# Kernel optimization log

Hardware: AMD Instinct MI355X
Metric: run time of the kernel (lower is better)

The kernel has to match this reference:

```python
import jax, jax.numpy as jnp
import numpy as np

GROUPS = 8
EPS = 1e-5


def setup_inputs() -> dict:
    key = jax.random.key(0)
    ks = jax.random.split(key, 7)
    b, c, h, w = 32, 256, 32, 32
    x = jax.random.normal(ks[0], (b, c, h, w), dtype=jnp.float32)
    gn_weight = jax.random.normal(ks[1], (c,), dtype=jnp.float32) * 0.02 + 1.0
    gn_bias = jax.random.normal(ks[2], (c,), dtype=jnp.float32) * 0.02
    w_qkv = jax.random.normal(ks[3], (3 * c, c), dtype=jnp.float32) / np.sqrt(c)
    b_qkv = jax.random.normal(ks[4], (3 * c,), dtype=jnp.float32) * 0.01
    w_out = jax.random.normal(ks[5], (c, c), dtype=jnp.float32) / np.sqrt(c)
    b_out = jax.random.normal(ks[6], (c,), dtype=jnp.float32) * 0.01
    return {"x": x, "gn_weight": gn_weight, "gn_bias": gn_bias,
            "w_qkv": w_qkv, "b_qkv": b_qkv, "w_out": w_out, "b_out": b_out}


def group_norm(x, weight, bias):
    b, c, h, w = x.shape
    xg = x.reshape(b, GROUPS, c // GROUPS, h, w)
    mean = jnp.mean(xg, axis=(2, 3, 4), keepdims=True)
    var = jnp.var(xg, axis=(2, 3, 4), keepdims=True)
    xg = (xg - mean) * jax.lax.rsqrt(var + EPS)
    x = xg.reshape(b, c, h, w)
    return x * weight[None, :, None, None] + bias[None, :, None, None]


def reference(x, gn_weight, gn_bias, w_qkv, b_qkv, w_out, b_out):
    b, c, h, w = x.shape
    x_norm = group_norm(x, gn_weight, gn_bias)
    # 1x1 conv == channel matmul: (b, 3c, h, w)
    qkv = jnp.einsum('oc,bchw->bohw', w_qkv, x_norm) + b_qkv[None, :, None, None]
    q, k, v = jnp.split(qkv, 3, axis=1)
    hw = h * w
    q = q.reshape(b, c, hw)  # used transposed: (b, hw, c)
    k = k.reshape(b, c, hw)
    v = v.reshape(b, c, hw)
    scale = 1.0 / jnp.sqrt(jnp.float32(c))
    attn = jax.nn.softmax(jnp.einsum('bcs,bct->bst', q, k) * scale, axis=-1)  # (b, hw, hw)
    out = jnp.einsum('bst,bct->bcs', attn, v).reshape(b, c, h, w)
    out = jnp.einsum('oc,bchw->bohw', w_out, out) + b_out[None, :, None, None]
    return out + x
```

## Files before the change

kernel.cpp:

```cpp
#include <hip/hip_runtime.h>
#include <hip/hip_bf16.h>


typedef __bf16 bf16x8 __attribute__((ext_vector_type(8)));
typedef __bf16 bf16x4 __attribute__((ext_vector_type(4)));
typedef float f32x4 __attribute__((ext_vector_type(4)));
typedef float f32x16 __attribute__((ext_vector_type(16)));

#define MFMA16(a, b, c) __builtin_amdgcn_mfma_f32_16x16x32_bf16(a, b, c, 0, 0, 0)
#define MFMA32(a, b, c) __builtin_amdgcn_mfma_f32_32x32x16_bf16(a, b, c, 0, 0, 0)

__global__ __launch_bounds__(256) void wconv_kernel(const float* __restrict__ wqkv,
                                                    const float* __restrict__ wout,
                                                    __bf16* __restrict__ wbf) {
    int idx = (blockIdx.x * 256 + threadIdx.x) * 8;
    const float* src = (idx < 196608) ? (wqkv + idx) : (wout + (idx - 196608));
    float4 v0 = *(const float4*)src;
    float4 v1 = *(const float4*)(src + 4);
    bf16x8 o;
    o[0] = (__bf16)v0.x; o[1] = (__bf16)v0.y; o[2] = (__bf16)v0.z; o[3] = (__bf16)v0.w;
    o[4] = (__bf16)v1.x; o[5] = (__bf16)v1.y; o[6] = (__bf16)v1.z; o[7] = (__bf16)v1.w;
    *(bf16x8*)&wbf[idx] = o;
}

__global__ __launch_bounds__(512) void gn_kernel(const float* __restrict__ x,
                                                 const float* __restrict__ gw,
                                                 const float* __restrict__ gb,
                                                 __bf16* __restrict__ xnT) {
    __shared__ float red[16];
    __shared__ float stats[2];
    __shared__ __bf16 Lds[512][40];
    const int b = blockIdx.x >> 3, g = blockIdx.x & 7;
    const size_t base = ((size_t)b * 256 + g * 32) * 1024;
    const float* xp = x + base;
    const int t = threadIdx.x;

    float s = 0.f, s2 = 0.f;
    #pragma unroll
    for (int i = 0; i < 8; i++) {
        int j = i * 512 + t;
        float4 v0 = *(const float4*)(xp + (size_t)j * 8);
        float4 v1 = *(const float4*)(xp + (size_t)j * 8 + 4);
        s  += v0.x + v0.y + v0.z + v0.w + v1.x + v1.y + v1.z + v1.w;
        s2 += v0.x*v0.x + v0.y*v0.y + v0.z*v0.z + v0.w*v0.w
            + v1.x*v1.x + v1.y*v1.y + v1.z*v1.z + v1.w*v1.w;
    }
    #pragma unroll
    for (int o = 32; o > 0; o >>= 1) { s += __shfl_down(s, o, 64); s2 += __shfl_down(s2, o, 64); }
    const int wv = t >> 6;
    if ((t & 63) == 0) { red[wv * 2] = s; red[wv * 2 + 1] = s2; }
    __syncthreads();
    if (t == 0) {
        float ts = 0.f, ts2 = 0.f;
        for (int w = 0; w < 8; w++) { ts += red[w * 2]; ts2 += red[w * 2 + 1]; }
        float mean = ts / 32768.f;
        float var = ts2 / 32768.f - mean * mean;
        stats[0] = mean; stats[1] = rsqrtf(var + 1e-5f);
    }
    __syncthreads();
    const float mean = stats[0], inv = stats[1];

    const int c = t >> 4;
    const int so = (t & 15) * 2;
    const float ga = gw[g * 32 + c], be = gb[g * 32 + c];

    for (int chunk = 0; chunk < 1024; chunk += 512) {
        #pragma unroll
        for (int i = 0; i < 16; i++) {
            int sl = so + i * 32;
            float2 v = *(const float2*)(xp + (size_t)c * 1024 + chunk + sl);
            Lds[sl][c]     = (__bf16)((v.x - mean) * inv * ga + be);
            Lds[sl + 1][c] = (__bf16)((v.y - mean) * inv * ga + be);
        }
        __syncthreads();
        {
            int sl = t;
            #pragma unroll
            for (int u = 0; u < 4; u++) {
                bf16x8 vv = *(const bf16x8*)&Lds[sl][u * 8];
                *(bf16x8*)&xnT[((size_t)b * 1024 + chunk + sl) * 256 + g * 32 + u * 8] = vv;
            }
        }
        __syncthreads();
    }
}

#define GEMM64_BODY(ArowBase_, BrowBase_)                                               \
    f32x4 acc[4][4] = {};                                                               \
    const int r_ = t >> 1, kc_ = (t & 1) * 32;                                          \
    bf16x8 pa[4], pb[4];                                                                \
    _Pragma("unroll")                                                                   \
    for (int u = 0; u < 4; u++) {                                                       \
        pa[u] = *(const bf16x8*)&(ArowBase_)[(size_t)r_ * 256 + kc_ + u * 8];           \
        pb[u] = *(const bf16x8*)&(BrowBase_)[(size_t)r_ * 256 + kc_ + u * 8];           \
    }                                                                                   \
    for (int kk = 0; kk < 256; kk += 64) {                                              \
        _Pragma("unroll")                                                               \
        for (int u = 0; u < 4; u++) {                                                   \
            *(bf16x8*)&As[r_][kc_ + u * 8] = pa[u];                                     \
            *(bf16x8*)&Bs[r_][kc_ + u * 8] = pb[u];                                     \
        }                                                                               \
        __syncthreads();                                                                \
        if (kk < 192) {                                                                 \
            _Pragma("unroll")                                                           \
            for (int u = 0; u < 4; u++) {                                               \
                pa[u] = *(const bf16x8*)&(ArowBase_)[(size_t)r_ * 256 + kk + 64 + kc_ + u * 8]; \
                pb[u] = *(const bf16x8*)&(BrowBase_)[(size_t)r_ * 256 + kk + 64 + kc_ + u * 8]; \
            }                                                                           \
        }                                                                               \
        _Pragma("unroll")                                                               \
        for (int kh = 0; kh < 2; kh++) {                                                \
            bf16x8 af[4], bfv[4];                                                       \
            _Pragma("unroll")                                                           \
            for (int im = 0; im < 4; im++)                                              \
                af[im] = *(const bf16x8*)&As[wm + im * 16 + l16][kh * 32 + quad * 8];   \
            _Pragma("unroll")                                                           \
            for (int in = 0; in < 4; in++)                                              \
                bfv[in] = *(const bf16x8*)&Bs[wn + in * 16 + l16][kh * 32 + quad * 8];  \
            _Pragma("unroll")                                                           \
            for (int im = 0; im < 4; im++)                                              \
                _Pragma("unroll")                                                       \
                for (int in = 0; in < 4; in++)                                          \
                    acc[im][in] = MFMA16(af[im], bfv[in], acc[im][in]);                 \
        }                                                                               \
        __syncthreads();                                                                \
    }

__global__ __launch_bounds__(256) void qkv_gemm(const __bf16* __restrict__ wbf,
                                                const float* __restrict__ bias,
                                                const __bf16* __restrict__ xnT,
                                                __bf16* __restrict__ qtr,
                                                __bf16* __restrict__ ktr,
                                                __bf16* __restrict__ vbuf) {
    __shared__ __bf16 As[128][72];
    __shared__ __bf16 Bs[128][72];
    const int b = blockIdx.z;
    const int n0 = blockIdx.x * 128, m0 = blockIdx.y * 128;
    const int t = threadIdx.x;
    const int wave = t >> 6, lane = t & 63, quad = lane >> 4, l16 = lane & 15;
    const int wm = (wave & 1) * 64, wn = (wave >> 1) * 64;
    const __bf16* arow = wbf + (size_t)m0 * 256;
    const __bf16* brow = xnT + ((size_t)b * 1024 + n0) * 256;

    GEMM64_BODY(arow, brow)

    #pragma unroll
    for (int im = 0; im < 4; im++) {
        #pragma unroll
        for (int in = 0; in < 4; in++) {
            int sg = n0 + wn + in * 16 + l16;
            int ob = m0 + wm + im * 16 + quad * 4;
            if (m0 < 512) {
                bf16x4 ov;
                #pragma unroll
                for (int r = 0; r < 4; r++) ov[r] = (__bf16)(acc[im][in][r] + bias[ob + r]);
                __bf16* dst = (m0 < 256) ? &qtr[((size_t)b * 1024 + sg) * 256 + ob]
                                         : &ktr[((size_t)b * 1024 + sg) * 256 + (ob - 256)];
                *(bf16x4*)dst = ov;
            } else {
                #pragma unroll
                for (int r = 0; r < 4; r++) {
                    float val = acc[im][in][r] + bias[ob + r];
                    vbuf[((size_t)b * 256 + (ob - 512 + r)) * 1024 + sg] = (__bf16)val;
                }
            }
        }
    }
}

__global__ __launch_bounds__(512, 2) void attn_kernel(const __bf16* __restrict__ qtr,
                                                      const __bf16* __restrict__ ktr,
                                                      const __bf16* __restrict__ vbuf,
                                                      __bf16* __restrict__ aoT) {
    __shared__ __bf16 Kt[2][32][260];
    __shared__ __bf16 Vs[2][256][36];
    __shared__ __bf16 Pl[4][32][72];
    __shared__ float Lred[4][2][32];
    const int b = blockIdx.x;
    const int tid = threadIdx.x;
    const int wave = tid >> 6, lane = tid & 63, half = lane >> 5, l31 = lane & 31;
    const int pair = wave & 3, th = wave >> 2;
    const int s0 = blockIdx.y * 128 + pair * 32;
    const float kscale = 0.09016844f;

    bf16x8 aq[16];
    #pragma unroll
    for (int ks = 0; ks < 16; ks++)
        aq[ks] = *(const bf16x8*)&qtr[((size_t)b * 1024 + s0 + l31) * 256 + ks * 16 + half * 8];

    const int k_row = tid >> 3;
    const int k_cb  = (tid & 7) * 8;
    const int v_c   = tid >> 1;
    const int v_th  = tid & 1;
    const size_t kbase = (size_t)b * 1024 * 256;
    const size_t vbase = (size_t)b * 256 * 1024;

    float l_part[16] = {};
    f32x16 o_acc[4] = {};

    for (int it = 0; it < 16; it++) {
        const int t0 = it * 64;
        #pragma unroll
        for (int u = 0; u < 4; u++) {
            bf16x8 kv = *(const bf16x8*)&ktr[kbase + (size_t)(t0 + k_row) * 256 + k_cb + u * 64];
            *(bf16x8*)&Kt[k_row >> 5][k_row & 31][k_cb + u * 64] = kv;
        }
        #pragma unroll
        for (int u = 0; u < 4; u++) {
            bf16x8 vv = *(const bf16x8*)&vbuf[vbase + (size_t)v_c * 1024 + t0 + v_th * 32 + u * 8];
            *(bf16x8*)&Vs[v_th][v_c][u * 8] = vv;
        }
        __syncthreads();

        f32x16 sc_a = {}, sc_b = {};
        #pragma unroll
        for (int ks = 0; ks < 8; ks++) {
            bf16x8 bk0 = *(const bf16x8*)&Kt[th][l31][ks * 16 + half * 8];
            bf16x8 bk1 = *(const bf16x8*)&Kt[th][l31][(ks + 8) * 16 + half * 8];
            sc_a = MFMA32(aq[ks], bk0, sc_a);
            sc_b = MFMA32(aq[ks + 8], bk1, sc_b);
        }
        #pragma unroll
        for (int r = 0; r < 16; r++) {
            float p = exp2f((sc_a[r] + sc_b[r]) * kscale);
            l_part[r] += p;
            int row = (r & 3) + 8 * (r >> 2) + 4 * half;
            Pl[pair][row][th * 32 + l31] = (__bf16)p;
        }
        __syncthreads();

        bf16x8 ap[4];
        #pragma unroll
        for (int kc = 0; kc < 4; kc++)
            ap[kc] = *(const bf16x8*)&Pl[pair][l31][kc * 16 + half * 8];
        #pragma unroll
        for (int n = 0; n < 4; n++) {
            int c = th * 128 + n * 32 + l31;
            #pragma unroll
            for (int kc = 0; kc < 4; kc++) {
                bf16x8 bv = *(const bf16x8*)&Vs[kc >> 1][c][(kc & 1) * 16 + half * 8];
                o_acc[n] = MFMA32(ap[kc], bv, o_acc[n]);
            }
        }
        __syncthreads();
    }

    float lsum[16];
    #pragma unroll
    for (int r = 0; r < 16; r++) {
        float l = l_part[r];
        #pragma unroll
        for (int m = 16; m > 0; m >>= 1) l += __shfl_xor(l, m, 32);
        lsum[r] = l;
        if (l31 == 0) {
            int row = (r & 3) + 8 * (r >> 2) + 4 * half;
            Lred[pair][th][row] = l;
        }
    }
    __syncthreads();
    #pragma unroll
    for (int r = 0; r < 16; r++) {
        int row = (r & 3) + 8 * (r >> 2) + 4 * half;
        float rinv = 1.0f / (lsum[r] + Lred[pair][1 - th][row]);
        #pragma unroll
        for (int n = 0; n < 4; n++) {
            int c = th * 128 + n * 32 + l31;
            aoT[((size_t)b * 1024 + s0 + row) * 256 + c] = (__bf16)(o_acc[n][r] * rinv);
        }
    }
}

__global__ __launch_bounds__(256) void proj_gemm(const __bf16* __restrict__ wbf_out,
                                                 const float* __restrict__ bias,
                                                 const __bf16* __restrict__ aoT,
                                                 const float* __restrict__ resid,
                                                 float* __restrict__ Out) {
    __shared__ __bf16 As[128][72];
    __shared__ __bf16 Bs[128][72];
    const int b = blockIdx.z;
    const int n0 = blockIdx.x * 128, m0 = blockIdx.y * 128;
    const int t = threadIdx.x;
    const int wave = t >> 6, lane = t & 63, quad = lane >> 4, l16 = lane & 15;
    const int wm = (wave & 1) * 64, wn = (wave >> 1) * 64;
    const __bf16* arow = wbf_out + (size_t)m0 * 256;
    const __bf16* brow = aoT + ((size_t)b * 1024 + n0) * 256;

    GEMM64_BODY(arow, brow)

    #pragma unroll
    for (int im = 0; im < 4; im++) {
        #pragma unroll
        for (int in = 0; in < 4; in++) {
            int sg = n0 + wn + in * 16 + l16;
            int ob = m0 + wm + im * 16 + quad * 4;
            #pragma unroll
            for (int r = 0; r < 4; r++) {
                int o = ob + r;
                size_t idx = ((size_t)b * 256 + o) * 1024 + sg;
                Out[idx] = acc[im][in][r] + bias[o] + resid[idx];
            }
        }
    }
}

extern "C" void kernel_launch(void* const* d_in, const int* in_sizes, int n_in,
                              void* d_out, int out_size, void* d_ws, size_t ws_size,
                              hipStream_t stream) {
    const float* x    = (const float*)d_in[0];
    const float* gw   = (const float*)d_in[1];
    const float* gb   = (const float*)d_in[2];
    const float* wqkv = (const float*)d_in[3];
    const float* bqkv = (const float*)d_in[4];
    const float* wout = (const float*)d_in[5];
    const float* bout = (const float*)d_in[6];
    float* out = (float*)d_out;

    const size_t T16 = (size_t)32 * 1024 * 256;
    __bf16* xnT  = (__bf16*)d_ws;
    __bf16* qtr  = xnT + T16;
    __bf16* ktr  = qtr + T16;
    __bf16* vbuf = ktr + T16;
    __bf16* aoT  = vbuf + T16;
    __bf16* wbf  = aoT + T16;

    wconv_kernel<<<dim3(128), 256, 0, stream>>>(wqkv, wout, wbf);
    gn_kernel<<<dim3(256), 512, 0, stream>>>(x, gw, gb, xnT);
    qkv_gemm<<<dim3(8, 6, 32), 256, 0, stream>>>(wbf, bqkv, xnT, qtr, ktr, vbuf);
    attn_kernel<<<dim3(32, 8), 512, 0, stream>>>(qtr, ktr, vbuf, aoT);
    proj_gemm<<<dim3(8, 2, 32), 256, 0, stream>>>(wbf + 196608, bout, aoT, x, out);
}
```

Before: 210.8 us.

## Fuse weight cast into groupnorm, stage GEMM epilogues through LDS, prefetch K/V

Folds the weight fp32-to-bf16 conversion into the groupnorm kernel, which removes one launch. The Q/K epilogue of the QKV GEMM and the projection epilogue are staged through shared memory so global stores (and residual loads) become coalesced 16-byte vectors. The attention loop prefetches the next K/V tile into registers while computing the current one, and raises wave priority around the MFMA sections. The added LDS round-trips and barriers in the epilogues, plus higher register pressure from the prefetch in attention, are the costs.

Measured after the change: 194.2 us. 7.9% less time.

```diff
diff --git a/kernel.cpp b/kernel.cpp
--- a/kernel.cpp
+++ b/kernel.cpp
@@ -4,29 +4,20 @@
 
 typedef __bf16 bf16x8 __attribute__((ext_vector_type(8)));
 typedef __bf16 bf16x4 __attribute__((ext_vector_type(4)));
+typedef __bf16 bf16x2 __attribute__((ext_vector_type(2)));
 typedef float f32x4 __attribute__((ext_vector_type(4)));
 typedef float f32x16 __attribute__((ext_vector_type(16)));
 
 #define MFMA16(a, b, c) __builtin_amdgcn_mfma_f32_16x16x32_bf16(a, b, c, 0, 0, 0)
 #define MFMA32(a, b, c) __builtin_amdgcn_mfma_f32_32x32x16_bf16(a, b, c, 0, 0, 0)
-
-__global__ __launch_bounds__(256) void wconv_kernel(const float* __restrict__ wqkv,
-                                                    const float* __restrict__ wout,
-                                                    __bf16* __restrict__ wbf) {
-    int idx = (blockIdx.x * 256 + threadIdx.x) * 8;
-    const float* src = (idx < 196608) ? (wqkv + idx) : (wout + (idx - 196608));
-    float4 v0 = *(const float4*)src;
-    float4 v1 = *(const float4*)(src + 4);
-    bf16x8 o;
-    o[0] = (__bf16)v0.x; o[1] = (__bf16)v0.y; o[2] = (__bf16)v0.z; o[3] = (__bf16)v0.w;
-    o[4] = (__bf16)v1.x; o[5] = (__bf16)v1.y; o[6] = (__bf16)v1.z; o[7] = (__bf16)v1.w;
-    *(bf16x8*)&wbf[idx] = o;
-}
 
 __global__ __launch_bounds__(512) void gn_kernel(const float* __restrict__ x,
                                                  const float* __restrict__ gw,
                                                  const float* __restrict__ gb,
-                                                 __bf16* __restrict__ xnT) {
+                                                 __bf16* __restrict__ xnT,
+                                                 const float* __restrict__ wqkv,
+                                                 const float* __restrict__ wout,
+                                                 __bf16* __restrict__ wbf) {
     __shared__ float red[16];
     __shared__ float stats[2];
     __shared__ __bf16 Lds[512][40];
@@ -34,6 +25,15 @@
     const size_t base = ((size_t)b * 256 + g * 32) * 1024;
     const float* xp = x + base;
     const int t = threadIdx.x;
+
+    {
+        int widx = (blockIdx.x * 512 + t) * 2;
+        const float* wsrc = (widx < 196608) ? (wqkv + widx) : (wout + (widx - 196608));
+        float2 wv = *(const float2*)wsrc;
+        bf16x2 wo;
+        wo[0] = (__bf16)wv.x; wo[1] = (__bf16)wv.y;
+        *(bf16x2*)&wbf[widx] = wo;
+    }
 
     float s = 0.f, s2 = 0.f;
     #pragma unroll
@@ -132,8 +132,10 @@
                                                 __bf16* __restrict__ qtr,
                                                 __bf16* __restrict__ ktr,
                                                 __bf16* __restrict__ vbuf) {
-    __shared__ __bf16 As[128][72];
-    __shared__ __bf16 Bs[128][72];
+    __shared__ union {
+        struct { __bf16 A[128][72]; __bf16 B[128][72]; } g;
+        __bf16 ct[128][136];
+    } sm;
     const int b = blockIdx.z;
     const int n0 = blockIdx.x * 128, m0 = blockIdx.y * 128;
     const int t = threadIdx.x;
@@ -141,23 +143,46 @@
     const int wm = (wave & 1) * 64, wn = (wave >> 1) * 64;
     const __bf16* arow = wbf + (size_t)m0 * 256;
     const __bf16* brow = xnT + ((size_t)b * 1024 + n0) * 256;
+    auto As = sm.g.A;
+    auto Bs = sm.g.B;
 
     GEMM64_BODY(arow, brow)
 
-    #pragma unroll
-    for (int im = 0; im < 4; im++) {
-        #pragma unroll
-        for (int in = 0; in < 4; in++) {
-            int sg = n0 + wn + in * 16 + l16;
-            int ob = m0 + wm + im * 16 + quad * 4;
-            if (m0 < 512) {
+    if (m0 < 512) {
+        #pragma unroll
+        for (int im = 0; im < 4; im++) {
+            #pragma unroll
+            for (int in = 0; in < 4; in++) {
+                int ob = m0 + wm + im * 16 + quad * 4;
                 bf16x4 ov;
                 #pragma unroll
                 for (int r = 0; r < 4; r++) ov[r] = (__bf16)(acc[im][in][r] + bias[ob + r]);
-                __bf16* dst = (m0 < 256) ? &qtr[((size_t)b * 1024 + sg) * 256 + ob]
-                                         : &ktr[((size_t)b * 1024 + sg) * 256 + (ob - 256)];
-                *(bf16x4*)dst = ov;
-            } else {
+                *(bf16x4*)&sm.ct[wn + in * 16 + l16][wm + im * 16 + quad * 4] = ov;
+            }
+        }
+        __syncthreads();
+        {
+            const int rbase = t >> 2, cf = t & 3;
+            #pragma unroll
+            for (int rr = 0; rr < 2; rr++) {
+                int row = rbase + rr * 64;
+                int sg = n0 + row;
+                __bf16* dst = (m0 < 256) ? &qtr[((size_t)b * 1024 + sg) * 256 + m0]
+                                         : &ktr[((size_t)b * 1024 + sg) * 256 + (m0 - 256)];
+                #pragma unroll
+                for (int u = 0; u < 4; u++) {
+                    int colb = cf * 8 + u * 32;
+                    *(bf16x8*)&dst[colb] = *(const bf16x8*)&sm.ct[row][colb];
+                }
+            }
+        }
+    } else {
+        #pragma unroll
+        for (int im = 0; im < 4; im++) {
+            #pragma unroll
+            for (int in = 0; in < 4; in++) {
+                int sg = n0 + wn + in * 16 + l16;
+                int ob = m0 + wm + im * 16 + quad * 4;
                 #pragma unroll
                 for (int r = 0; r < 4; r++) {
                     float val = acc[im][in][r] + bias[ob + r];
@@ -198,21 +223,31 @@
     float l_part[16] = {};
     f32x16 o_acc[4] = {};
 
+    bf16x8 kpre[4], vpre[4];
+    #pragma unroll
+    for (int u = 0; u < 4; u++) {
+        kpre[u] = *(const bf16x8*)&ktr[kbase + (size_t)k_row * 256 + k_cb + u * 64];
+        vpre[u] = *(const bf16x8*)&vbuf[vbase + (size_t)v_c * 1024 + v_th * 32 + u * 8];
+    }
+
     for (int it = 0; it < 16; it++) {
-        const int t0 = it * 64;
         #pragma unroll
         for (int u = 0; u < 4; u++) {
-            bf16x8 kv = *(const bf16x8*)&ktr[kbase + (size_t)(t0 + k_row) * 256 + k_cb + u * 64];
-            *(bf16x8*)&Kt[k_row >> 5][k_row & 31][k_cb + u * 64] = kv;
-        }
-        #pragma unroll
-        for (int u = 0; u < 4; u++) {
-            bf16x8 vv = *(const bf16x8*)&vbuf[vbase + (size_t)v_c * 1024 + t0 + v_th * 32 + u * 8];
-            *(bf16x8*)&Vs[v_th][v_c][u * 8] = vv;
-        }
-        __syncthreads();
+            *(bf16x8*)&Kt[k_row >> 5][k_row & 31][k_cb + u * 64] = kpre[u];
+            *(bf16x8*)&Vs[v_th][v_c][u * 8] = vpre[u];
+        }
+        __syncthreads();
+        if (it < 15) {
+            const int t1 = (it + 1) * 64;
+            #pragma unroll
+            for (int u = 0; u < 4; u++) {
+                kpre[u] = *(const bf16x8*)&ktr[kbase + (size_t)(t1 + k_row) * 256 + k_cb + u * 64];
+                vpre[u] = *(const bf16x8*)&vbuf[vbase + (size_t)v_c * 1024 + t1 + v_th * 32 + u * 8];
+            }
+        }
 
         f32x16 sc_a = {}, sc_b = {};
+        __builtin_amdgcn_s_setprio(1);
         #pragma unroll
         for (int ks = 0; ks < 8; ks++) {
             bf16x8 bk0 = *(const bf16x8*)&Kt[th][l31][ks * 16 + half * 8];
@@ -220,6 +255,7 @@
             sc_a = MFMA32(aq[ks], bk0, sc_a);
             sc_b = MFMA32(aq[ks + 8], bk1, sc_b);
         }
+        __builtin_amdgcn_s_setprio(0);
         #pragma unroll
         for (int r = 0; r < 16; r++) {
             float p = exp2f((sc_a[r] + sc_b[r]) * kscale);
@@ -233,6 +269,7 @@
         #pragma unroll
         for (int kc = 0; kc < 4; kc++)
             ap[kc] = *(const bf16x8*)&Pl[pair][l31][kc * 16 + half * 8];
+        __builtin_amdgcn_s_setprio(1);
         #pragma unroll
         for (int n = 0; n < 4; n++) {
             int c = th * 128 + n * 32 + l31;
@@ -242,6 +279,7 @@
                 o_acc[n] = MFMA32(ap[kc], bv, o_acc[n]);
             }
         }
+        __builtin_amdgcn_s_setprio(0);
         __syncthreads();
     }
 
@@ -275,8 +313,10 @@
                                                  const __bf16* __restrict__ aoT,
                                                  const float* __restrict__ resid,
                                                  float* __restrict__ Out) {
-    __shared__ __bf16 As[128][72];
-    __shared__ __bf16 Bs[128][72];
+    __shared__ union {
+        struct { __bf16 A[128][72]; __bf16 B[128][72]; } g;
+        float cf[64][132];
+    } sm;
     const int b = blockIdx.z;
     const int n0 = blockIdx.x * 128, m0 = blockIdx.y * 128;
     const int t = threadIdx.x;
@@ -284,22 +324,42 @@
     const int wm = (wave & 1) * 64, wn = (wave >> 1) * 64;
     const __bf16* arow = wbf_out + (size_t)m0 * 256;
     const __bf16* brow = aoT + ((size_t)b * 1024 + n0) * 256;
+    auto As = sm.g.A;
+    auto Bs = sm.g.B;
 
     GEMM64_BODY(arow, brow)
 
-    #pragma unroll
-    for (int im = 0; im < 4; im++) {
-        #pragma unroll
-        for (int in = 0; in < 4; in++) {
-            int sg = n0 + wn + in * 16 + l16;
-            int ob = m0 + wm + im * 16 + quad * 4;
-            #pragma unroll
-            for (int r = 0; r < 4; r++) {
-                int o = ob + r;
-                size_t idx = ((size_t)b * 256 + o) * 1024 + sg;
-                Out[idx] = acc[im][in][r] + bias[o] + resid[idx];
-            }
-        }
+    for (int h = 0; h < 2; h++) {
+        if ((wave & 1) == h) {
+            #pragma unroll
+            for (int im = 0; im < 4; im++)
+                #pragma unroll
+                for (int in = 0; in < 4; in++)
+                    #pragma unroll
+                    for (int r = 0; r < 4; r++)
+                        sm.cf[im * 16 + quad * 4 + r][wn + in * 16 + l16] = acc[im][in][r];
+        }
+        __syncthreads();
+        {
+            const int rloc = t >> 2, cq = (t & 3) * 4;
+            const int o = m0 + h * 64 + rloc;
+            const float bo = bias[o];
+            const float* rrow = &resid[((size_t)b * 256 + o) * 1024 + n0];
+            float* orow = &Out[((size_t)b * 256 + o) * 1024 + n0];
+            #pragma unroll
+            for (int u = 0; u < 8; u++) {
+                int col = cq + u * 16;
+                f32x4 cv = *(const f32x4*)&sm.cf[rloc][col];
+                float4 rv = *(const float4*)&rrow[col];
+                float4 ov;
+                ov.x = cv[0] + bo + rv.x;
+                ov.y = cv[1] + bo + rv.y;
+                ov.z = cv[2] + bo + rv.z;
+                ov.w = cv[3] + bo + rv.w;
+                *(float4*)&orow[col] = ov;
+            }
+        }
+        __syncthreads();
     }
 }
 
@@ -323,8 +383,7 @@
     __bf16* aoT  = vbuf + T16;
     __bf16* wbf  = aoT + T16;
 
-    wconv_kernel<<<dim3(128), 256, 0, stream>>>(wqkv, wout, wbf);
-    gn_kernel<<<dim3(256), 512, 0, stream>>>(x, gw, gb, xnT);
+    gn_kernel<<<dim3(256), 512, 0, stream>>>(x, gw, gb, xnT, wqkv, wout, wbf);
     qkv_gemm<<<dim3(8, 6, 32), 256, 0, stream>>>(wbf, bqkv, xnT, qtr, ktr, vbuf);
     attn_kernel<<<dim3(32, 8), 512, 0, stream>>>(qtr, ktr, vbuf, aoT);
     proj_gemm<<<dim3(8, 2, 32), 256, 0, stream>>>(wbf + 196608, bout, aoT, x, out);
```
